# Performance work log

Measured on AMD Instinct MI355X. Metric: run time of the kernel, lower is better.

The kernel has to match this reference:

```python
import jax, jax.numpy as jnp
import numpy as np

B, N, C = 8, 1024, 768
DIM_HEAD = 32
NUM_HEADS = C // DIM_HEAD  # 24


def setup_inputs() -> dict:
    key = jax.random.key(0)
    ks = jax.random.split(key, 6)
    s = 0.02
    return {
        "x": jax.random.normal(ks[0], (B, N, C), dtype=jnp.float32),
        "shared_rel_pos": jax.random.normal(ks[1], (NUM_HEADS, N, N), dtype=jnp.float32),
        "Wqkv": jax.random.normal(ks[2], (3 * C, C), dtype=jnp.float32) * s,
        "bqkv": jax.random.normal(ks[3], (3 * C,), dtype=jnp.float32) * s,
        "Wproj": jax.random.normal(ks[4], (C, C), dtype=jnp.float32) * s,
        "bproj": jax.random.normal(ks[5], (C,), dtype=jnp.float32) * s,
    }


def reference(x, shared_rel_pos, Wqkv, bqkv, Wproj, bproj):
    b, n, c = x.shape
    h, dh = NUM_HEADS, DIM_HEAD
    scale = dh ** -0.5
    # qkv projection: [B,N,3C] -> view as [B,N,H,3*dh] (head_first layout)
    qkv = (jnp.einsum('bnc,oc->bno', x, Wqkv) + bqkv).reshape(b, n, h, 3 * dh)
    qkv = jnp.transpose(qkv, (0, 2, 1, 3))          # [B,H,N,3*dh]
    q, k, v = jnp.split(qkv, 3, axis=-1)            # each [B,H,N,dh]
    attn = jnp.einsum('bhqd,bhkd->bhqk', q * scale, k)  # [B,H,N,N]
    attn = attn + shared_rel_pos[None]              # broadcast bias [H,N,N]
    attn = jax.nn.softmax(attn, axis=-1)
    out = jnp.einsum('bhqk,bhkd->bhqd', attn, v)    # [B,H,N,dh]
    out = jnp.transpose(out, (0, 2, 1, 3)).reshape(b, n, h * dh)
    return jnp.einsum('bnc,oc->bno', out, Wproj) + bproj
```

## Files before the change

kernel.cpp:

```cpp
#include <hip/hip_runtime.h>

typedef __bf16 bf16_t;
typedef __bf16 bf16x8 __attribute__((ext_vector_type(8)));
typedef __bf16 bf16x4 __attribute__((ext_vector_type(4)));
typedef float f32x4 __attribute__((ext_vector_type(4)));

#define MFMA16(a, b, c) __builtin_amdgcn_mfma_f32_16x16x32_bf16(a, b, c, 0, 0, 0)

__device__ __forceinline__ void g2l16(const void* g, void* l) {
  __builtin_amdgcn_global_load_lds(
      (__attribute__((address_space(1))) void*)g,
      (__attribute__((address_space(3))) void*)l, 16, 0, 0);
}

__global__ void cvt_f32_bf16(const float* __restrict__ in, bf16_t* __restrict__ out, int n4) {
  int i = blockIdx.x * blockDim.x + threadIdx.x;
  if (i >= n4) return;
  const float4 v = ((const float4*)in)[i];
  bf16x4 o;
  o[0] = (bf16_t)v.x; o[1] = (bf16_t)v.y; o[2] = (bf16_t)v.z; o[3] = (bf16_t)v.w;
  ((bf16x4*)out)[i] = o;
}

__global__ void transpose_v(const bf16_t* __restrict__ Vb, bf16_t* __restrict__ Vtb) {
  __shared__ bf16_t T[64][40];
  const int bh = blockIdx.y, s0 = blockIdx.x * 64;
  const int r = threadIdx.x >> 2, c8 = (threadIdx.x & 3) * 8;
  const bf16x8 v = *(const bf16x8*)(Vb + ((size_t)bh * 1024 + s0 + r) * 32 + c8);
#pragma unroll
  for (int j = 0; j < 8; ++j) T[r][c8 + j] = v[j];
  __syncthreads();
  const int d = threadIdx.x >> 3, q8 = (threadIdx.x & 7) * 8;
  bf16x8 o;
#pragma unroll
  for (int j = 0; j < 8; ++j) o[j] = T[q8 + j][d];
  *(bf16x8*)(Vtb + ((size_t)bh * 32 + d) * 1024 + s0 + q8) = o;
}

template <int MODE>
__global__ __launch_bounds__(256, 2) void gemm_bt(
    const bf16_t* __restrict__ A, const bf16_t* __restrict__ Bw,
    const float* __restrict__ bias, float* __restrict__ Cout,
    bf16_t* __restrict__ Qb, bf16_t* __restrict__ Kb, bf16_t* __restrict__ Vb,
    int M, int N, int K) {
  __shared__ bf16_t As[128 * 32];
  __shared__ bf16_t Bs[128 * 32];
  const int tid = threadIdx.x;
  const int wave = tid >> 6, lane = tid & 63, quad = lane >> 4, lr = lane & 15;
  const int bm = blockIdx.x * 128, bn = blockIdx.y * 128;
  const int wm = (wave >> 1) * 64, wn = (wave & 1) * 64;

  f32x4 acc[4][4] = {};

  const bf16_t* Ag;
  size_t strideA64;
  if (MODE == 0) {
    Ag = A + (size_t)(bm + (tid >> 2)) * K + (tid & 3) * 8;
    strideA64 = (size_t)64 * K;
  } else {
    const int rr = bm + (tid >> 2);
    const int bidx = rr >> 10, seq = rr & 1023;
    Ag = A + ((size_t)bidx * 24 * 1024 + seq) * 32 + (tid & 3) * 8;
    strideA64 = (size_t)64 * 32;
  }
  const bf16_t* Bg = Bw + (size_t)(bn + (tid >> 2)) * K + (tid & 3) * 8;
  bf16_t* As0 = As + tid * 8;
  bf16_t* Bs0 = Bs + tid * 8;
  const size_t strideB64 = (size_t)64 * K;

  for (int k0 = 0; k0 < K; k0 += 32) {
    const size_t aoff = (MODE == 0) ? (size_t)k0 : (size_t)(k0 >> 5) * 32768;
    __syncthreads();
    g2l16(Ag + aoff, As0);
    g2l16(Ag + strideA64 + aoff, As0 + 2048);
    g2l16(Bg + k0, Bs0);
    g2l16(Bg + strideB64 + k0, Bs0 + 2048);
    __syncthreads();
    bf16x8 af[4], bfr[4];
#pragma unroll
    for (int i = 0; i < 4; ++i)
      af[i] = *(const bf16x8*)(As + (wm + i * 16 + lr) * 32 + quad * 8);
#pragma unroll
    for (int j = 0; j < 4; ++j)
      bfr[j] = *(const bf16x8*)(Bs + (wn + j * 16 + lr) * 32 + quad * 8);
#pragma unroll
    for (int i = 0; i < 4; ++i)
#pragma unroll
      for (int j = 0; j < 4; ++j)
        acc[i][j] = MFMA16(af[i], bfr[j], acc[i][j]);
  }

#pragma unroll
  for (int i = 0; i < 4; ++i) {
    const int row = bm + wm + i * 16 + quad * 4;
#pragma unroll
    for (int j = 0; j < 4; ++j) {
      const int col = bn + wn + j * 16 + lr;
      const float bb = bias[col];
#pragma unroll
      for (int r = 0; r < 4; ++r) {
        const float v = acc[i][j][r] + bb;
        const int rr = row + r;
        if (MODE == 1) {
          Cout[(size_t)rr * N + col] = v;
        } else {
          const int b = rr >> 10, seq = rr & 1023;
          const int head = col / 96, w = col % 96;
          const int bh = b * 24 + head;
          if (w < 32) {
            Qb[((size_t)bh * 1024 + seq) * 32 + w] = (bf16_t)(v * 0.17677669529663687f);
          } else if (w < 64) {
            Kb[((size_t)bh * 1024 + seq) * 32 + (w - 32)] = (bf16_t)v;
          } else {
            Vb[((size_t)bh * 1024 + seq) * 32 + (w - 64)] = (bf16_t)v;
          }
        }
      }
    }
  }
}

__global__ __launch_bounds__(256, 4) void attn_flash(
    const bf16_t* __restrict__ Qb, const bf16_t* __restrict__ Kb,
    const bf16_t* __restrict__ Vtb, const float* __restrict__ rel,
    bf16_t* __restrict__ Ob) {
  __shared__ bf16_t Ps[4][16 * 132];

  const int tid = threadIdx.x;
  const int wave = tid >> 6, lane = tid & 63, quad = lane >> 4, lr = lane & 15;

  const int flat = blockIdx.x;
  const int xcd = flat & 7, slot = flat >> 3;
  const int pair = xcd + 8 * (slot >> 4);
  const int qi = slot & 15;
  const int b = pair / 24, h = pair % 24;
  const int bh = b * 24 + h;
  const int q0 = qi * 64 + wave * 16;
  const float LOG2E = 1.44269504f;

  const bf16x8 qf = *(const bf16x8*)(Qb + ((size_t)bh * 1024 + q0 + lr) * 32 + quad * 8);

  f32x4 o_acc[2] = {};
  float l_i[4] = {0.f, 0.f, 0.f, 0.f};

  const float* relg = rel + ((size_t)h * 1024 + q0 + quad * 4) * 1024 + lr;
  const bf16_t* Kg = Kb + (size_t)bh * 1024 * 32;
  const bf16_t* Vg = Vtb + (size_t)bh * 32 * 1024;
  bf16_t* Pw = &Ps[wave][0];

  auto body = [&](int kt) {
    float bv[8][4];
    const float* rb = relg + kt;
#pragma unroll
    for (int jt = 0; jt < 8; ++jt)
#pragma unroll
      for (int r = 0; r < 4; ++r)
        bv[jt][r] = rb[(size_t)r * 1024 + jt * 16] * LOG2E;

    const bf16_t* Kbase = Kg + (size_t)kt * 32;
    const bf16_t* Vbase = Vg + kt;

    f32x4 s[8];
    const f32x4 zz = {0.f, 0.f, 0.f, 0.f};
#pragma unroll
    for (int jt = 0; jt < 8; ++jt) {
      const bf16x8 kf = *(const bf16x8*)(Kbase + (size_t)(jt * 16 + lr) * 32 + quad * 8);
      s[jt] = MFMA16(qf, kf, zz);
    }
#pragma unroll
    for (int jt = 0; jt < 8; ++jt)
#pragma unroll
      for (int r = 0; r < 4; ++r)
        s[jt][r] = exp2f(fmaf(s[jt][r], LOG2E, bv[jt][r]));

#pragma unroll
    for (int jt = 0; jt < 8; ++jt)
#pragma unroll
      for (int r = 0; r < 4; ++r)
        Pw[(quad * 4 + r) * 132 + jt * 16 + lr] = (bf16_t)s[jt][r];

#pragma unroll
    for (int r = 0; r < 4; ++r) {
      float sm = 0.f;
#pragma unroll
      for (int jt = 0; jt < 8; ++jt) sm += s[jt][r];
#pragma unroll
      for (int off = 1; off < 16; off <<= 1) sm += __shfl_xor(sm, off, 16);
      l_i[r] += sm;
    }

#pragma unroll
    for (int ks = 0; ks < 4; ++ks) {
      const bf16x8 pf = *(const bf16x8*)(Pw + lr * 132 + ks * 32 + quad * 8);
#pragma unroll
      for (int nt = 0; nt < 2; ++nt) {
        const bf16x8 vf = *(const bf16x8*)(Vbase + (size_t)(nt * 16 + lr) * 1024 + ks * 32 + quad * 8);
        o_acc[nt] = MFMA16(pf, vf, o_acc[nt]);
      }
    }
  };

  for (int kt = 0; kt < 1024; kt += 256) {
    body(kt);
    body(kt + 128);
  }

  float inv_l[4];
#pragma unroll
  for (int r = 0; r < 4; ++r) inv_l[r] = 1.0f / l_i[r];
#pragma unroll
  for (int nt = 0; nt < 2; ++nt)
#pragma unroll
    for (int r = 0; r < 4; ++r) {
      const int seq = q0 + quad * 4 + r;
      Ob[((size_t)bh * 1024 + seq) * 32 + nt * 16 + lr] = (bf16_t)(o_acc[nt][r] * inv_l[r]);
    }
}

extern "C" void kernel_launch(void* const* d_in, const int* in_sizes, int n_in,
                              void* d_out, int out_size, void* d_ws, size_t ws_size,
                              hipStream_t stream) {
  const float* x = (const float*)d_in[0];
  const float* rel = (const float*)d_in[1];
  const float* Wqkv = (const float*)d_in[2];
  const float* bqkv = (const float*)d_in[3];
  const float* Wproj = (const float*)d_in[4];
  const float* bproj = (const float*)d_in[5];
  float* out = (float*)d_out;

  char* ws = (char*)d_ws;
  bf16_t* xb = (bf16_t*)ws;     ws += (size_t)8192 * 768 * 2;
  bf16_t* wqkvb = (bf16_t*)ws;  ws += (size_t)2304 * 768 * 2;
  bf16_t* wprojb = (bf16_t*)ws; ws += (size_t)768 * 768 * 2;
  bf16_t* Qb = (bf16_t*)ws;     ws += (size_t)192 * 1024 * 32 * 2;
  bf16_t* Kb = (bf16_t*)ws;     ws += (size_t)192 * 1024 * 32 * 2;
  bf16_t* Vb = (bf16_t*)ws;     ws += (size_t)192 * 1024 * 32 * 2;
  bf16_t* Vtb = (bf16_t*)ws;    ws += (size_t)192 * 1024 * 32 * 2;
  bf16_t* Ob = xb;

  cvt_f32_bf16<<<(8192 * 768 / 4 + 255) / 256, 256, 0, stream>>>(x, xb, 8192 * 768 / 4);
  cvt_f32_bf16<<<(2304 * 768 / 4 + 255) / 256, 256, 0, stream>>>(Wqkv, wqkvb, 2304 * 768 / 4);
  cvt_f32_bf16<<<(768 * 768 / 4 + 255) / 256, 256, 0, stream>>>(Wproj, wprojb, 768 * 768 / 4);

  gemm_bt<0><<<dim3(64, 18), 256, 0, stream>>>(xb, wqkvb, bqkv, nullptr,
                                               Qb, Kb, Vb, 8192, 2304, 768);
  transpose_v<<<dim3(16, 192), 256, 0, stream>>>(Vb, Vtb);
  attn_flash<<<dim3(3072), 256, 0, stream>>>(Qb, Kb, Vtb, rel, Ob);
  gemm_bt<1><<<dim3(64, 6), 256, 0, stream>>>(Ob, wprojb, bproj, out,
                                              nullptr, nullptr, nullptr, 8192, 768, 768);
}
```

Measured before the change: 396.8 us.

## Prefetch rel-pos bias tiles, defer row-sum shuffles, fuse conversion launches

The attention kernel now double-buffers the relative-position bias loads, issuing the next 128-key tile's global loads before computing the current tile, so the bias fetch latency overlaps the MFMA and exp work. The per-tile cross-lane shuffle reduction of the softmax denominator moves to a single reduction at the end. Launch bounds drop from 4 to 3 blocks per SM to leave room for the extra bias registers. The three fp32-to-bf16 conversion kernels are merged into one launch. The cost is higher register pressure and lower occupancy in the attention kernel.

```diff
diff --git a/kernel.cpp b/kernel.cpp
--- a/kernel.cpp
+++ b/kernel.cpp
@@ -13,13 +13,27 @@
       (__attribute__((address_space(3))) void*)l, 16, 0, 0);
 }
 
-__global__ void cvt_f32_bf16(const float* __restrict__ in, bf16_t* __restrict__ out, int n4) {
-  int i = blockIdx.x * blockDim.x + threadIdx.x;
-  if (i >= n4) return;
-  const float4 v = ((const float4*)in)[i];
+__global__ void cvt3_f32_bf16(const float* __restrict__ a, bf16_t* __restrict__ oa, int na4,
+                              const float* __restrict__ b, bf16_t* __restrict__ ob, int nb4,
+                              const float* __restrict__ c, bf16_t* __restrict__ oc, int nc4) {
+  int j = blockIdx.x * blockDim.x + threadIdx.x;
+  const float* in;
+  bf16_t* out;
+  if (j < na4) {
+    in = a; out = oa;
+  } else {
+    j -= na4;
+    if (j < nb4) { in = b; out = ob; }
+    else {
+      j -= nb4;
+      if (j >= nc4) return;
+      in = c; out = oc;
+    }
+  }
+  const float4 v = ((const float4*)in)[j];
   bf16x4 o;
   o[0] = (bf16_t)v.x; o[1] = (bf16_t)v.y; o[2] = (bf16_t)v.z; o[3] = (bf16_t)v.w;
-  ((bf16x4*)out)[i] = o;
+  ((bf16x4*)out)[j] = o;
 }
 
 __global__ void transpose_v(const bf16_t* __restrict__ Vb, bf16_t* __restrict__ Vtb) {
@@ -120,7 +134,7 @@
   }
 }
 
-__global__ __launch_bounds__(256, 4) void attn_flash(
+__global__ __launch_bounds__(256, 3) void attn_flash(
     const bf16_t* __restrict__ Qb, const bf16_t* __restrict__ Kb,
     const bf16_t* __restrict__ Vtb, const float* __restrict__ rel,
     bf16_t* __restrict__ Ob) {
@@ -141,22 +155,23 @@
   const bf16x8 qf = *(const bf16x8*)(Qb + ((size_t)bh * 1024 + q0 + lr) * 32 + quad * 8);
 
   f32x4 o_acc[2] = {};
-  float l_i[4] = {0.f, 0.f, 0.f, 0.f};
+  float lsum[4] = {0.f, 0.f, 0.f, 0.f};
 
   const float* relg = rel + ((size_t)h * 1024 + q0 + quad * 4) * 1024 + lr;
   const bf16_t* Kg = Kb + (size_t)bh * 1024 * 32;
   const bf16_t* Vg = Vtb + (size_t)bh * 32 * 1024;
   bf16_t* Pw = &Ps[wave][0];
 
-  auto body = [&](int kt) {
-    float bv[8][4];
+  auto loadbias = [&](int kt, float (&bv)[8][4]) {
     const float* rb = relg + kt;
 #pragma unroll
     for (int jt = 0; jt < 8; ++jt)
 #pragma unroll
       for (int r = 0; r < 4; ++r)
         bv[jt][r] = rb[(size_t)r * 1024 + jt * 16] * LOG2E;
-
+  };
+
+  auto body = [&](int kt, const float (&bv)[8][4]) {
     const bf16_t* Kbase = Kg + (size_t)kt * 32;
     const bf16_t* Vbase = Vg + kt;
 
@@ -184,9 +199,7 @@
       float sm = 0.f;
 #pragma unroll
       for (int jt = 0; jt < 8; ++jt) sm += s[jt][r];
-#pragma unroll
-      for (int off = 1; off < 16; off <<= 1) sm += __shfl_xor(sm, off, 16);
-      l_i[r] += sm;
+      lsum[r] += sm;
     }
 
 #pragma unroll
@@ -200,14 +213,24 @@
     }
   };
 
+  float bv0[8][4], bv1[8][4];
+  loadbias(0, bv0);
+#pragma unroll 2
   for (int kt = 0; kt < 1024; kt += 256) {
-    body(kt);
-    body(kt + 128);
+    loadbias(kt + 128, bv1);
+    body(kt, bv0);
+    if (kt + 256 < 1024) loadbias(kt + 256, bv0);
+    body(kt + 128, bv1);
   }
 
   float inv_l[4];
 #pragma unroll
-  for (int r = 0; r < 4; ++r) inv_l[r] = 1.0f / l_i[r];
+  for (int r = 0; r < 4; ++r) {
+    float sm = lsum[r];
+#pragma unroll
+    for (int off = 1; off < 16; off <<= 1) sm += __shfl_xor(sm, off, 16);
+    inv_l[r] = 1.0f / sm;
+  }
 #pragma unroll
   for (int nt = 0; nt < 2; ++nt)
 #pragma unroll
@@ -238,9 +261,9 @@
   bf16_t* Vtb = (bf16_t*)ws;    ws += (size_t)192 * 1024 * 32 * 2;
   bf16_t* Ob = xb;
 
-  cvt_f32_bf16<<<(8192 * 768 / 4 + 255) / 256, 256, 0, stream>>>(x, xb, 8192 * 768 / 4);
-  cvt_f32_bf16<<<(2304 * 768 / 4 + 255) / 256, 256, 0, stream>>>(Wqkv, wqkvb, 2304 * 768 / 4);
-  cvt_f32_bf16<<<(768 * 768 / 4 + 255) / 256, 256, 0, stream>>>(Wproj, wprojb, 768 * 768 / 4);
+  const int na4 = 8192 * 768 / 4, nb4 = 2304 * 768 / 4, nc4 = 768 * 768 / 4;
+  cvt3_f32_bf16<<<(na4 + nb4 + nc4 + 255) / 256, 256, 0, stream>>>(
+      x, xb, na4, Wqkv, wqkvb, nb4, Wproj, wprojb, nc4);
 
   gemm_bt<0><<<dim3(64, 18), 256, 0, stream>>>(xb, wqkvb, bqkv, nullptr,
                                                Qb, Kb, Vb, 8192, 2304, 768);
```

New measurement: 473.7 us. 1.19x slower.
